# Kernel tuning notes

Hardware: AMD Instinct MI355X
Metric: run time of the kernel (lower is better)

The kernel has to match this reference:

```python
import jax, jax.numpy as jnp
import numpy as np

D = 512      # feature_bins
DK = 64      # d_k = d_v
H = 8        # n_heads
EPS = 1e-5


def setup_inputs() -> dict:
    key = jax.random.key(0)
    ks = jax.random.split(key, 12)
    B, S = 4, 2048
    s = 1.0 / np.sqrt(D)
    inp = {
        "Q": jax.random.normal(ks[0], (B, S, D), jnp.float32),
        "K": jax.random.normal(ks[1], (B, S, D), jnp.float32),
        "V": jax.random.normal(ks[2], (B, S, D), jnp.float32),
        # nn.Linear params: weight [out, in], bias [out]
        "Wq": jax.random.normal(ks[3], (H * DK, D), jnp.float32) * s,
        "bq": jnp.zeros((H * DK,), jnp.float32),
        "Wk": jax.random.normal(ks[4], (H * DK, D), jnp.float32) * s,
        "bk": jnp.zeros((H * DK,), jnp.float32),
        "Wv": jax.random.normal(ks[5], (H * DK, D), jnp.float32) * s,
        "bv": jnp.zeros((H * DK,), jnp.float32),
        "Wo": jax.random.normal(ks[6], (D, H * DK), jnp.float32) * s,
        "bo": jnp.zeros((D,), jnp.float32),
        "gamma": jnp.ones((D,), jnp.float32),
        "beta": jnp.zeros((D,), jnp.float32),
    }
    return inp


def _layernorm(x, gamma, beta):
    mu = jnp.mean(x, axis=-1, keepdims=True)
    var = jnp.mean(jnp.square(x - mu), axis=-1, keepdims=True)
    return (x - mu) * jax.lax.rsqrt(var + EPS) * gamma + beta


def reference(Q, K, V, Wq, bq, Wk, bk, Wv, bv, Wo, bo, gamma, beta):
    B, S, _ = Q.shape
    residual = Q
    # projections -> [B, H, S, DK]
    q = (Q @ Wq.T + bq).reshape(B, S, H, DK).transpose(0, 2, 1, 3)
    k = (K @ Wk.T + bk).reshape(B, S, H, DK).transpose(0, 2, 1, 3)
    v = (V @ Wv.T + bv).reshape(B, S, H, DK).transpose(0, 2, 1, 3)
    # NOTE: original code has NO 1/sqrt(d_k) scaling
    scores = jnp.einsum("bhqd,bhkd->bhqk", q, k)
    attn = jax.nn.softmax(scores, axis=-1)
    context = jnp.einsum("bhqk,bhkd->bhqd", attn, v)
    context = context.transpose(0, 2, 1, 3).reshape(B, S, H * DK)
    output = context @ Wo.T + bo
    out = _layernorm(output + residual, gamma, beta)
    return (out, attn)
```

## Files before the change

### kernel.cpp

```cpp
#include <hip/hip_runtime.h>

#define NB 4
#define NS 2048
#define ND 512
#define NH 8
#define NDK 64
#define LN_EPS 1e-5f
#define SCLAMP 115.0f
#define LOG2E 1.44269504f

typedef __attribute__((ext_vector_type(8))) short short8;
typedef __attribute__((ext_vector_type(4))) short s16x4;
typedef __attribute__((ext_vector_type(4))) float f32x4;

__device__ inline short f2bf(float x) {
    unsigned u = __builtin_bit_cast(unsigned, x);
    unsigned r = (u + 0x7FFFu + ((u >> 16) & 1u)) >> 16;
    return (short)r;
}
__device__ inline float bf2f(short h) {
    unsigned u = ((unsigned)(unsigned short)h) << 16;
    return __builtin_bit_cast(float, u);
}
__device__ inline unsigned splitT(float x) {
    unsigned u = __builtin_bit_cast(unsigned, x);
    unsigned h = u >> 16;
    float r = x - bf2f((short)h);
    unsigned l = __builtin_bit_cast(unsigned, r) >> 16;
    return (h & 0xFFFFu) | (l << 16);
}

__device__ inline int swzS(int row, int b8) {
    return row * 64 + (((b8) * 8) ^ ((row & 7) << 3));
}
__device__ inline int swz4(int row, int g4) {
    return row * 64 + ((((g4 >> 1)) * 8) ^ ((row & 7) << 3)) + (g4 & 1) * 4;
}

__global__ __launch_bounds__(256) void k_projm_all(
    const float* __restrict__ Qx, const float* __restrict__ Kx,
    const float* __restrict__ Vx,
    const float* __restrict__ Wq, const float* __restrict__ bq,
    const float* __restrict__ Wk, const float* __restrict__ bk,
    const float* __restrict__ Wv, const float* __restrict__ bv,
    short* __restrict__ qh, short* __restrict__ ql,
    short* __restrict__ kh, short* __restrict__ kl,
    short* __restrict__ vtb)
{
    __shared__ short WsH[8192], WsL[8192];
    const int which = blockIdx.z;
    const float* X    = which == 0 ? Qx : (which == 1 ? Kx : Vx);
    const float* W    = which == 0 ? Wq : (which == 1 ? Wk : Wv);
    const float* bias = which == 0 ? bq : (which == 1 ? bk : bv);
    short* outh       = which == 0 ? qh : (which == 1 ? kh : vtb);
    short* outl       = which == 0 ? ql : kl;

    const int tid = threadIdx.x;
    const int w = tid >> 6, lane = tid & 63;
    const int lr = lane & 15, lg = lane >> 4;
    const int row0 = blockIdx.y * 64;
    const int col0 = blockIdx.x * 128;
    const int xrow = row0 + w * 16 + lr;

    f32x4 acc[8] = {};

    float4 wb[8], ab[4];
#pragma unroll
    for (int i = 0; i < 8; ++i) {
        int idx = tid + 256 * i, wrow = idx >> 4, g4 = idx & 15;
        wb[i] = *(const float4*)&W[(size_t)(col0 + wrow) * ND + g4 * 4];
    }
#pragma unroll
    for (int ks = 0; ks < 2; ++ks) {
        ab[2*ks+0] = *(const float4*)&X[(size_t)xrow * ND + ks * 32 + lg * 8];
        ab[2*ks+1] = *(const float4*)&X[(size_t)xrow * ND + ks * 32 + lg * 8 + 4];
    }

    for (int kc = 0; kc < 8; ++kc) {
        __syncthreads();
#pragma unroll
        for (int i = 0; i < 8; ++i) {
            int idx = tid + 256 * i, wrow = idx >> 4, g4 = idx & 15;
            s16x4 hv, lv;
            unsigned p0 = splitT(wb[i].x), p1 = splitT(wb[i].y);
            unsigned p2 = splitT(wb[i].z), p3 = splitT(wb[i].w);
            hv[0] = (short)p0; lv[0] = (short)(p0 >> 16);
            hv[1] = (short)p1; lv[1] = (short)(p1 >> 16);
            hv[2] = (short)p2; lv[2] = (short)(p2 >> 16);
            hv[3] = (short)p3; lv[3] = (short)(p3 >> 16);
            int off = swz4(wrow, g4);
            *(s16x4*)&WsH[off] = hv;
            *(s16x4*)&WsL[off] = lv;
        }
        __syncthreads();

        short8 ah[2], al[2];
#pragma unroll
        for (int ks = 0; ks < 2; ++ks) {
#pragma unroll
            for (int j = 0; j < 4; ++j) {
                unsigned p = splitT(ab[2*ks][j]);
                ah[ks][j] = (short)p; al[ks][j] = (short)(p >> 16);
            }
#pragma unroll
            for (int j = 0; j < 4; ++j) {
                unsigned p = splitT(ab[2*ks+1][j]);
                ah[ks][4+j] = (short)p; al[ks][4+j] = (short)(p >> 16);
            }
        }

        if (kc < 7) {
            const int kn = (kc + 1) * 64;
#pragma unroll
            for (int i = 0; i < 8; ++i) {
                int idx = tid + 256 * i, wrow = idx >> 4, g4 = idx & 15;
                wb[i] = *(const float4*)&W[(size_t)(col0 + wrow) * ND + kn + g4 * 4];
            }
#pragma unroll
            for (int ks = 0; ks < 2; ++ks) {
                ab[2*ks+0] = *(const float4*)&X[(size_t)xrow * ND + kn + ks * 32 + lg * 8];
                ab[2*ks+1] = *(const float4*)&X[(size_t)xrow * ND + kn + ks * 32 + lg * 8 + 4];
            }
        }

#pragma unroll
        for (int cs = 0; cs < 8; ++cs)
#pragma unroll
            for (int ks = 0; ks < 2; ++ks) {
                short8 fh = *(const short8*)&WsH[swzS(cs * 16 + lr, ks * 4 + lg)];
                short8 fl = *(const short8*)&WsL[swzS(cs * 16 + lr, ks * 4 + lg)];
                acc[cs] = __builtin_amdgcn_mfma_f32_16x16x32_bf16(ah[ks], fh, acc[cs], 0, 0, 0);
                acc[cs] = __builtin_amdgcn_mfma_f32_16x16x32_bf16(ah[ks], fl, acc[cs], 0, 0, 0);
                acc[cs] = __builtin_amdgcn_mfma_f32_16x16x32_bf16(al[ks], fh, acc[cs], 0, 0, 0);
            }
    }

#pragma unroll
    for (int cs = 0; cs < 8; ++cs) {
        int c = col0 + cs * 16 + lr;
        int h_ = c >> 6, dk = c & (NDK - 1);
        float bv = bias[c];
#pragma unroll
        for (int r = 0; r < 4; ++r) {
            int gr = row0 + w * 16 + lg * 4 + r;
            int b_ = gr >> 11, s_ = gr & (NS - 1);
            float x = acc[cs][r] + bv;
            if (which == 0) x *= LOG2E;
            if (which != 2) {
                size_t idx = (((size_t)b_ * NH + h_) * NS + s_) * NDK + dk;
                short hb = f2bf(x);
                outh[idx] = hb;
                outl[idx] = f2bf(x - bf2f(hb));
            } else {
                size_t idx = (((size_t)b_ * NH + h_) * NDK + dk) * NS + s_;
                outh[idx] = f2bf(x);
            }
        }
    }
}

__device__ inline void att_decode2(int wg, int& bh, int& rt) {
    rt = (wg >> 3) & 15;
    bh = (wg & 7) + ((wg >> 7) << 3);
}

__global__ __launch_bounds__(256) void k_att(
    const short* __restrict__ qh, const short* __restrict__ ql,
    const short* __restrict__ kh, const short* __restrict__ kl,
    const short* __restrict__ vtb,
    short* __restrict__ ctxb, float* __restrict__ attn)
{
    __shared__ short KsH[4096], KsL[4096], Vs[4096];
    __shared__ short plbf[4][32][72];
    const int tid = threadIdx.x;
    const int w = tid >> 6, lane = tid & 63;
    const int lr = lane & 15, lg = lane >> 4;
    int bh, rt;
    att_decode2(blockIdx.x, bh, rt);
    const int row0 = rt * 128 + w * 16;
    const size_t base = (size_t)bh * NS * NDK;
    const short* vb = vtb + (size_t)bh * NDK * NS;
    float* ab = attn + (size_t)bh * NS * NS;
    const int srow0 = tid >> 3, sb8 = tid & 7;
    const int srow1 = srow0 + 32;

    short8 ah[2][2], al[2][2];
#pragma unroll
    for (int st = 0; st < 2; ++st)
#pragma unroll
        for (int ks = 0; ks < 2; ++ks) {
            size_t idx = base + (size_t)(row0 + st * 64 + lr) * NDK + ks * 32 + lg * 8;
            ah[st][ks] = *(const short8*)&qh[idx];
            al[st][ks] = *(const short8*)&ql[idx];
        }

    float lsum[2][4] = {};
    f32x4 vacc[2][4] = {};

    short8 nh0, nh1, nl0, nl1, nv0, nv1;
    {
        nh0 = *(const short8*)&kh[base + (size_t)(srow0) * NDK + sb8 * 8];
        nh1 = *(const short8*)&kh[base + (size_t)(srow1) * NDK + sb8 * 8];
        nl0 = *(const short8*)&kl[base + (size_t)(srow0) * NDK + sb8 * 8];
        nl1 = *(const short8*)&kl[base + (size_t)(srow1) * NDK + sb8 * 8];
        nv0 = *(const short8*)&vb[(size_t)srow0 * NS + sb8 * 8];
        nv1 = *(const short8*)&vb[(size_t)srow1 * NS + sb8 * 8];
    }

    for (int c = 0; c < 32; ++c) {
        short8 ch0 = nh0, ch1 = nh1, cl0 = nl0, cl1 = nl1, cv0 = nv0, cv1 = nv1;
        __syncthreads();
        *(short8*)&KsH[swzS(srow0, sb8)] = ch0;
        *(short8*)&KsH[swzS(srow1, sb8)] = ch1;
        *(short8*)&KsL[swzS(srow0, sb8)] = cl0;
        *(short8*)&KsL[swzS(srow1, sb8)] = cl1;
        *(short8*)&Vs[swzS(srow0, sb8)] = cv0;
        *(short8*)&Vs[swzS(srow1, sb8)] = cv1;
        __syncthreads();

        if (c < 31) {
            const int coln = (c + 1) * 64;
            nh0 = *(const short8*)&kh[base + (size_t)(coln + srow0) * NDK + sb8 * 8];
            nh1 = *(const short8*)&kh[base + (size_t)(coln + srow1) * NDK + sb8 * 8];
            nl0 = *(const short8*)&kl[base + (size_t)(coln + srow0) * NDK + sb8 * 8];
            nl1 = *(const short8*)&kl[base + (size_t)(coln + srow1) * NDK + sb8 * 8];
            nv0 = *(const short8*)&vb[(size_t)srow0 * NS + coln + sb8 * 8];
            nv1 = *(const short8*)&vb[(size_t)srow1 * NS + coln + sb8 * 8];
        }

        f32x4 sa[2][4] = {};
#pragma unroll
        for (int cs = 0; cs < 4; ++cs)
#pragma unroll
            for (int ks = 0; ks < 2; ++ks) {
                short8 fh = *(const short8*)&KsH[swzS(cs * 16 + lr, ks * 4 + lg)];
                short8 fl = *(const short8*)&KsL[swzS(cs * 16 + lr, ks * 4 + lg)];
#pragma unroll
                for (int st = 0; st < 2; ++st) {
                    sa[st][cs] = __builtin_amdgcn_mfma_f32_16x16x32_bf16(ah[st][ks], fh, sa[st][cs], 0, 0, 0);
                    sa[st][cs] = __builtin_amdgcn_mfma_f32_16x16x32_bf16(ah[st][ks], fl, sa[st][cs], 0, 0, 0);
                    sa[st][cs] = __builtin_amdgcn_mfma_f32_16x16x32_bf16(al[st][ks], fh, sa[st][cs], 0, 0, 0);
                }
            }

#pragma unroll
        for (int st = 0; st < 2; ++st)
#pragma unroll
            for (int cs = 0; cs < 4; ++cs)
#pragma unroll
                for (int r = 0; r < 4; ++r) {
                    float e = __builtin_amdgcn_exp2f(fminf(sa[st][cs][r], SCLAMP));
                    lsum[st][r] += e;
                    plbf[w][st * 16 + lg * 4 + r][cs * 16 + lr] = f2bf(e);
                }

#pragma unroll
        for (int k2 = 0; k2 < 2; ++k2) {
            short8 pa0 = *(const short8*)&plbf[w][lr][k2 * 32 + lg * 8];
            short8 pa1 = *(const short8*)&plbf[w][16 + lr][k2 * 32 + lg * 8];
#pragma unroll
            for (int d = 0; d < 4; ++d) {
                short8 vf = *(const short8*)&Vs[swzS(d * 16 + lr, k2 * 4 + lg)];
                vacc[0][d] = __builtin_amdgcn_mfma_f32_16x16x32_bf16(pa0, vf, vacc[0][d], 0, 0, 0);
                vacc[1][d] = __builtin_amdgcn_mfma_f32_16x16x32_bf16(pa1, vf, vacc[1][d], 0, 0, 0);
            }
        }
    }

#pragma unroll
    for (int st = 0; st < 2; ++st)
#pragma unroll
        for (int r = 0; r < 4; ++r)
#pragma unroll
            for (int off = 1; off < 16; off <<= 1)
                lsum[st][r] += __shfl_xor(lsum[st][r], off);

    float iL[2][4];
#pragma unroll
    for (int st = 0; st < 2; ++st)
#pragma unroll
        for (int r = 0; r < 4; ++r) iL[st][r] = 1.0f / lsum[st][r];

    const int b_ = bh >> 3, h_ = bh & 7;
#pragma unroll
    for (int st = 0; st < 2; ++st)
#pragma unroll
        for (int d = 0; d < 4; ++d)
#pragma unroll
            for (int r = 0; r < 4; ++r) {
                int row = row0 + st * 64 + lg * 4 + r;
                ctxb[((size_t)b_ * NS + row) * ND + h_ * NDK + d * 16 + lr] =
                    f2bf(vacc[st][d][r] * iL[st][r]);
            }

    {
        nh0 = *(const short8*)&kh[base + (size_t)(srow0) * NDK + sb8 * 8];
        nh1 = *(const short8*)&kh[base + (size_t)(srow1) * NDK + sb8 * 8];
        nl0 = *(const short8*)&kl[base + (size_t)(srow0) * NDK + sb8 * 8];
        nl1 = *(const short8*)&kl[base + (size_t)(srow1) * NDK + sb8 * 8];
    }

    for (int c = 0; c < 32; ++c) {
        short8 ch0 = nh0, ch1 = nh1, cl0 = nl0, cl1 = nl1;
        __syncthreads();
        *(short8*)&KsH[swzS(srow0, sb8)] = ch0;
        *(short8*)&KsH[swzS(srow1, sb8)] = ch1;
        *(short8*)&KsL[swzS(srow0, sb8)] = cl0;
        *(short8*)&KsL[swzS(srow1, sb8)] = cl1;
        __syncthreads();

        if (c < 31) {
            const int coln = (c + 1) * 64;
            nh0 = *(const short8*)&kh[base + (size_t)(coln + srow0) * NDK + sb8 * 8];
            nh1 = *(const short8*)&kh[base + (size_t)(coln + srow1) * NDK + sb8 * 8];
            nl0 = *(const short8*)&kl[base + (size_t)(coln + srow0) * NDK + sb8 * 8];
            nl1 = *(const short8*)&kl[base + (size_t)(coln + srow1) * NDK + sb8 * 8];
        }

        const int col0 = c * 64;
        f32x4 sa[2][4] = {};
#pragma unroll
        for (int cs = 0; cs < 4; ++cs)
#pragma unroll
            for (int ks = 0; ks < 2; ++ks) {
                short8 fh = *(const short8*)&KsH[swzS(cs * 16 + lr, ks * 4 + lg)];
                short8 fl = *(const short8*)&KsL[swzS(cs * 16 + lr, ks * 4 + lg)];
#pragma unroll
                for (int st = 0; st < 2; ++st) {
                    sa[st][cs] = __builtin_amdgcn_mfma_f32_16x16x32_bf16(ah[st][ks], fh, sa[st][cs], 0, 0, 0);
                    sa[st][cs] = __builtin_amdgcn_mfma_f32_16x16x32_bf16(ah[st][ks], fl, sa[st][cs], 0, 0, 0);
                    sa[st][cs] = __builtin_amdgcn_mfma_f32_16x16x32_bf16(al[st][ks], fh, sa[st][cs], 0, 0, 0);
                }
            }

#pragma unroll
        for (int st = 0; st < 2; ++st)
#pragma unroll
            for (int cs = 0; cs < 4; ++cs)
#pragma unroll
                for (int r = 0; r < 4; ++r) {
                    float p = __builtin_amdgcn_exp2f(fminf(sa[st][cs][r], SCLAMP)) * iL[st][r];
                    ab[(size_t)(row0 + st * 64 + lg * 4 + r) * NS + col0 + cs * 16 + lr] = p;
                }
    }
}

__global__ __launch_bounds__(256) void k_outproj_m(
    const short* __restrict__ Xc, const float* __restrict__ W,
    const float* __restrict__ bias, const float* __restrict__ Qin,
    float* __restrict__ out)
{
    __shared__ short WsH[8192], WsL[8192];
    const int tid = threadIdx.x;
    const int w = tid >> 6, lane = tid & 63;
    const int lr = lane & 15, lg = lane >> 4;
    const int row0 = blockIdx.y * 64;
    const int col0 = blockIdx.x * 128;
    const int xrow = row0 + w * 16 + lr;

    f32x4 acc[8] = {};

    float4 wb[8];
    short8 abn[2];
#pragma unroll
    for (int i = 0; i < 8; ++i) {
        int idx = tid + 256 * i, wrow = idx >> 4, g4 = idx & 15;
        wb[i] = *(const float4*)&W[(size_t)(col0 + wrow) * ND + g4 * 4];
    }
#pragma unroll
    for (int ks = 0; ks < 2; ++ks)
        abn[ks] = *(const short8*)&Xc[(size_t)xrow * ND + ks * 32 + lg * 8];

    for (int kc = 0; kc < 8; ++kc) {
        __syncthreads();
#pragma unroll
        for (int i = 0; i < 8; ++i) {
            int idx = tid + 256 * i, wrow = idx >> 4, g4 = idx & 15;
            s16x4 hv, lv;
            unsigned p0 = splitT(wb[i].x), p1 = splitT(wb[i].y);
            unsigned p2 = splitT(wb[i].z), p3 = splitT(wb[i].w);
            hv[0] = (short)p0; lv[0] = (short)(p0 >> 16);
            hv[1] = (short)p1; lv[1] = (short)(p1 >> 16);
            hv[2] = (short)p2; lv[2] = (short)(p2 >> 16);
            hv[3] = (short)p3; lv[3] = (short)(p3 >> 16);
            int off = swz4(wrow, g4);
            *(s16x4*)&WsH[off] = hv;
            *(s16x4*)&WsL[off] = lv;
        }
        __syncthreads();

        short8 ah[2] = { abn[0], abn[1] };

        if (kc < 7) {
            const int kn = (kc + 1) * 64;
#pragma unroll
            for (int i = 0; i < 8; ++i) {
                int idx = tid + 256 * i, wrow = idx >> 4, g4 = idx & 15;
                wb[i] = *(const float4*)&W[(size_t)(col0 + wrow) * ND + kn + g4 * 4];
            }
#pragma unroll
            for (int ks = 0; ks < 2; ++ks)
                abn[ks] = *(const short8*)&Xc[(size_t)xrow * ND + kn + ks * 32 + lg * 8];
        }

#pragma unroll
        for (int cs = 0; cs < 8; ++cs)
#pragma unroll
            for (int ks = 0; ks < 2; ++ks) {
                short8 fh = *(const short8*)&WsH[swzS(cs * 16 + lr, ks * 4 + lg)];
                short8 fl = *(const short8*)&WsL[swzS(cs * 16 + lr, ks * 4 + lg)];
                acc[cs] = __builtin_amdgcn_mfma_f32_16x16x32_bf16(ah[ks], fh, acc[cs], 0, 0, 0);
                acc[cs] = __builtin_amdgcn_mfma_f32_16x16x32_bf16(ah[ks], fl, acc[cs], 0, 0, 0);
            }
    }

#pragma unroll
    for (int cs = 0; cs < 8; ++cs) {
        int c = col0 + cs * 16 + lr;
        float bv = bias[c];
#pragma unroll
        for (int r = 0; r < 4; ++r) {
            int gr = row0 + w * 16 + lg * 4 + r;
            float res = Qin[(size_t)gr * ND + c];
            out[(size_t)gr * ND + c] = acc[cs][r] + bv + res;
        }
    }
}

__global__ __launch_bounds__(256) void k_ln(
    float* __restrict__ out, const float* __restrict__ gamma,
    const float* __restrict__ beta)
{
    const int tid = threadIdx.x;
    float* p = out + (size_t)blockIdx.x * ND;
    float2 v = *(const float2*)&p[tid * 2];

    float s = v.x + v.y;
#pragma unroll
    for (int off = 32; off > 0; off >>= 1) s += __shfl_xor(s, off);
    __shared__ float red1[4];
    __shared__ float red2[4];
    if ((tid & 63) == 0) red1[tid >> 6] = s;
    __syncthreads();
    const float mu = (red1[0] + red1[1] + red1[2] + red1[3]) * (1.0f / ND);

    float dx = v.x - mu, dy = v.y - mu;
    float q = dx * dx + dy * dy;
#pragma unroll
    for (int off = 32; off > 0; off >>= 1) q += __shfl_xor(q, off);
    if ((tid & 63) == 0) red2[tid >> 6] = q;
    __syncthreads();
    const float var = (red2[0] + red2[1] + red2[2] + red2[3]) * (1.0f / ND);
    const float inv = rsqrtf(var + LN_EPS);

    float2 g = *(const float2*)&gamma[tid * 2];
    float2 be = *(const float2*)&beta[tid * 2];
    float2 o = { dx * inv * g.x + be.x, dy * inv * g.y + be.y };
    *(float2*)&p[tid * 2] = o;
}

extern "C" void kernel_launch(void* const* d_in, const int* in_sizes, int n_in,
                              void* d_out, int out_size, void* d_ws, size_t ws_size,
                              hipStream_t stream)
{
    const float* Q    = (const float*)d_in[0];
    const float* K    = (const float*)d_in[1];
    const float* V    = (const float*)d_in[2];
    const float* Wq   = (const float*)d_in[3];
    const float* bq   = (const float*)d_in[4];
    const float* Wk   = (const float*)d_in[5];
    const float* bk   = (const float*)d_in[6];
    const float* Wv   = (const float*)d_in[7];
    const float* bv   = (const float*)d_in[8];
    const float* Wo   = (const float*)d_in[9];
    const float* bo   = (const float*)d_in[10];
    const float* gam  = (const float*)d_in[11];
    const float* bet  = (const float*)d_in[12];

    float* out  = (float*)d_out;
    float* attn = out + (size_t)NB * NS * ND;

    const size_t QKV = (size_t)NB * NH * NS * NDK;
    short* qh   = (short*)d_ws;
    short* ql   = qh + QKV;
    short* kh   = ql + QKV;
    short* kl   = kh + QKV;
    short* vtb  = kl + QKV;
    short* ctxb = vtb + QKV;

    dim3 blk(256);

    dim3 gP(ND / 128, (NB * NS) / 64, 3);
    k_projm_all<<<gP, blk, 0, stream>>>(Q, K, V, Wq, bq, Wk, bk, Wv, bv,
                                        qh, ql, kh, kl, vtb);

    dim3 gAtt((NS / 128) * NB * NH);
    k_att<<<gAtt, blk, 0, stream>>>(qh, ql, kh, kl, vtb, ctxb, attn);

    dim3 gO(ND / 128, (NB * NS) / 64);
    k_outproj_m<<<gO, blk, 0, stream>>>(ctxb, Wo, bo, Q, out);

    k_ln<<<dim3(NB * NS), blk, 0, stream>>>(out, gam, bet);
}
```

Measured before the change: 307.2 us.

## Double-buffer K/V shared tiles in attention and drop exp clamp

Converts the attention kernel's K/V shared-memory tiles to double buffers with prefetch two chunks ahead. This removes one barrier per iteration, so global loads and LDS stores overlap MFMA compute. It also removes the fminf clamp before exp2, which saves an instruction per score but risks overflow if scores exceed the fp32 exp range. The double buffers add LDS usage and may lower occupancy.

```diff
diff --git a/kernel.cpp b/kernel.cpp
--- a/kernel.cpp
+++ b/kernel.cpp
@@ -6,7 +6,6 @@
 #define NH 8
 #define NDK 64
 #define LN_EPS 1e-5f
-#define SCLAMP 115.0f
 #define LOG2E 1.44269504f
 
 typedef __attribute__((ext_vector_type(8))) short short8;
@@ -170,7 +169,7 @@
     const short* __restrict__ vtb,
     short* __restrict__ ctxb, float* __restrict__ attn)
 {
-    __shared__ short KsH[4096], KsL[4096], Vs[4096];
+    __shared__ short KsH[2][4096], KsL[2][4096], Vs[2][4096];
     __shared__ short plbf[4][32][72];
     const int tid = threadIdx.x;
     const int w = tid >> 6, lane = tid & 63;
@@ -183,6 +182,7 @@
     float* ab = attn + (size_t)bh * NS * NS;
     const int srow0 = tid >> 3, sb8 = tid & 7;
     const int srow1 = srow0 + 32;
+    const int so0 = swzS(srow0, sb8), so1 = swzS(srow1, sb8);
 
     short8 ah[2][2], al[2][2];
 #pragma unroll
@@ -198,28 +198,32 @@
     f32x4 vacc[2][4] = {};
 
     short8 nh0, nh1, nl0, nl1, nv0, nv1;
-    {
-        nh0 = *(const short8*)&kh[base + (size_t)(srow0) * NDK + sb8 * 8];
-        nh1 = *(const short8*)&kh[base + (size_t)(srow1) * NDK + sb8 * 8];
-        nl0 = *(const short8*)&kl[base + (size_t)(srow0) * NDK + sb8 * 8];
-        nl1 = *(const short8*)&kl[base + (size_t)(srow1) * NDK + sb8 * 8];
-        nv0 = *(const short8*)&vb[(size_t)srow0 * NS + sb8 * 8];
-        nv1 = *(const short8*)&vb[(size_t)srow1 * NS + sb8 * 8];
-    }
+    nh0 = *(const short8*)&kh[base + (size_t)(srow0) * NDK + sb8 * 8];
+    nh1 = *(const short8*)&kh[base + (size_t)(srow1) * NDK + sb8 * 8];
+    nl0 = *(const short8*)&kl[base + (size_t)(srow0) * NDK + sb8 * 8];
+    nl1 = *(const short8*)&kl[base + (size_t)(srow1) * NDK + sb8 * 8];
+    nv0 = *(const short8*)&vb[(size_t)srow0 * NS + sb8 * 8];
+    nv1 = *(const short8*)&vb[(size_t)srow1 * NS + sb8 * 8];
+    *(short8*)&KsH[0][so0] = nh0;  *(short8*)&KsH[0][so1] = nh1;
+    *(short8*)&KsL[0][so0] = nl0;  *(short8*)&KsL[0][so1] = nl1;
+    *(short8*)&Vs[0][so0]  = nv0;  *(short8*)&Vs[0][so1]  = nv1;
+    nh0 = *(const short8*)&kh[base + (size_t)(64 + srow0) * NDK + sb8 * 8];
+    nh1 = *(const short8*)&kh[base + (size_t)(64 + srow1) * NDK + sb8 * 8];
+    nl0 = *(const short8*)&kl[base + (size_t)(64 + srow0) * NDK + sb8 * 8];
+    nl1 = *(const short8*)&kl[base + (size_t)(64 + srow1) * NDK + sb8 * 8];
+    nv0 = *(const short8*)&vb[(size_t)srow0 * NS + 64 + sb8 * 8];
+    nv1 = *(const short8*)&vb[(size_t)srow1 * NS + 64 + sb8 * 8];
 
     for (int c = 0; c < 32; ++c) {
-        short8 ch0 = nh0, ch1 = nh1, cl0 = nl0, cl1 = nl1, cv0 = nv0, cv1 = nv1;
+        const int cur = c & 1, nxt = cur ^ 1;
         __syncthreads();
-        *(short8*)&KsH[swzS(srow0, sb8)] = ch0;
-        *(short8*)&KsH[swzS(srow1, sb8)] = ch1;
-        *(short8*)&KsL[swzS(srow0, sb8)] = cl0;
-        *(short8*)&KsL[swzS(srow1, sb8)] = cl1;
-        *(short8*)&Vs[swzS(srow0, sb8)] = cv0;
-        *(short8*)&Vs[swzS(srow1, sb8)] = cv1;
-        __syncthreads();
-
         if (c < 31) {
-            const int coln = (c + 1) * 64;
+            *(short8*)&KsH[nxt][so0] = nh0;  *(short8*)&KsH[nxt][so1] = nh1;
+            *(short8*)&KsL[nxt][so0] = nl0;  *(short8*)&KsL[nxt][so1] = nl1;
+            *(short8*)&Vs[nxt][so0]  = nv0;  *(short8*)&Vs[nxt][so1]  = nv1;
+        }
+        if (c < 30) {
+            const int coln = (c + 2) * 64;
             nh0 = *(const short8*)&kh[base + (size_t)(coln + srow0) * NDK + sb8 * 8];
             nh1 = *(const short8*)&kh[base + (size_t)(coln + srow1) * NDK + sb8 * 8];
             nl0 = *(const short8*)&kl[base + (size_t)(coln + srow0) * NDK + sb8 * 8];
@@ -233,8 +237,8 @@
         for (int cs = 0; cs < 4; ++cs)
 #pragma unroll
             for (int ks = 0; ks < 2; ++ks) {
-                short8 fh = *(const short8*)&KsH[swzS(cs * 16 + lr, ks * 4 + lg)];
-                short8 fl = *(const short8*)&KsL[swzS(cs * 16 + lr, ks * 4 + lg)];
+                short8 fh = *(const short8*)&KsH[cur][swzS(cs * 16 + lr, ks * 4 + lg)];
+                short8 fl = *(const short8*)&KsL[cur][swzS(cs * 16 + lr, ks * 4 + lg)];
 #pragma unroll
                 for (int st = 0; st < 2; ++st) {
                     sa[st][cs] = __builtin_amdgcn_mfma_f32_16x16x32_bf16(ah[st][ks], fh, sa[st][cs], 0, 0, 0);
@@ -249,7 +253,7 @@
             for (int cs = 0; cs < 4; ++cs)
 #pragma unroll
                 for (int r = 0; r < 4; ++r) {
-                    float e = __builtin_amdgcn_exp2f(fminf(sa[st][cs][r], SCLAMP));
+                    float e = __builtin_amdgcn_exp2f(sa[st][cs][r]);
                     lsum[st][r] += e;
                     plbf[w][st * 16 + lg * 4 + r][cs * 16 + lr] = f2bf(e);
                 }
@@ -260,7 +264,7 @@
             short8 pa1 = *(const short8*)&plbf[w][16 + lr][k2 * 32 + lg * 8];
 #pragma unroll
             for (int d = 0; d < 4; ++d) {
-                short8 vf = *(const short8*)&Vs[swzS(d * 16 + lr, k2 * 4 + lg)];
+                short8 vf = *(const short8*)&Vs[cur][swzS(d * 16 + lr, k2 * 4 + lg)];
                 vacc[0][d] = __builtin_amdgcn_mfma_f32_16x16x32_bf16(pa0, vf, vacc[0][d], 0, 0, 0);
                 vacc[1][d] = __builtin_amdgcn_mfma_f32_16x16x32_bf16(pa1, vf, vacc[1][d], 0, 0, 0);
             }
@@ -293,24 +297,27 @@
                     f2bf(vacc[st][d][r] * iL[st][r]);
             }
 
-    {
-        nh0 = *(const short8*)&kh[base + (size_t)(srow0) * NDK + sb8 * 8];
-        nh1 = *(const short8*)&kh[base + (size_t)(srow1) * NDK + sb8 * 8];
-        nl0 = *(const short8*)&kl[base + (size_t)(srow0) * NDK + sb8 * 8];
-        nl1 = *(const short8*)&kl[base + (size_t)(srow1) * NDK + sb8 * 8];
-    }
+    nh0 = *(const short8*)&kh[base + (size_t)(srow0) * NDK + sb8 * 8];
+    nh1 = *(const short8*)&kh[base + (size_t)(srow1) * NDK + sb8 * 8];
+    nl0 = *(const short8*)&kl[base + (size_t)(srow0) * NDK + sb8 * 8];
+    nl1 = *(const short8*)&kl[base + (size_t)(srow1) * NDK + sb8 * 8];
+    __syncthreads();
+    *(short8*)&KsH[0][so0] = nh0;  *(short8*)&KsH[0][so1] = nh1;
+    *(short8*)&KsL[0][so0] = nl0;  *(short8*)&KsL[0][so1] = nl1;
+    nh0 = *(const short8*)&kh[base + (size_t)(64 + srow0) * NDK + sb8 * 8];
+    nh1 = *(const short8*)&kh[base + (size_t)(64 + srow1) * NDK + sb8 * 8];
+    nl0 = *(const short8*)&kl[base + (size_t)(64 + srow0) * NDK + sb8 * 8];
+    nl1 = *(const short8*)&kl[base + (size_t)(64 + srow1) * NDK + sb8 * 8];
 
     for (int c = 0; c < 32; ++c) {
-        short8 ch0 = nh0, ch1 = nh1, cl0 = nl0, cl1 = nl1;
+        const int cur = c & 1, nxt = cur ^ 1;
         __syncthreads();
-        *(short8*)&KsH[swzS(srow0, sb8)] = ch0;
-        *(short8*)&KsH[swzS(srow1, sb8)] = ch1;
-        *(short8*)&KsL[swzS(srow0, sb8)] = cl0;
-        *(short8*)&KsL[swzS(srow1, sb8)] = cl1;
-        __syncthreads();
-
         if (c < 31) {
-            const int coln = (c + 1) * 64;
+            *(short8*)&KsH[nxt][so0] = nh0;  *(short8*)&KsH[nxt][so1] = nh1;
+            *(short8*)&KsL[nxt][so0] = nl0;  *(short8*)&KsL[nxt][so1] = nl1;
+        }
+        if (c < 30) {
+            const int coln = (c + 2) * 64;
             nh0 = *(const short8*)&kh[base + (size_t)(coln + srow0) * NDK + sb8 * 8];
             nh1 = *(const short8*)&kh[base + (size_t)(coln + srow1) * NDK + sb8 * 8];
             nl0 = *(const short8*)&kl[base + (size_t)(coln + srow0) * NDK + sb8 * 8];
@@ -323,8 +330,8 @@
         for (int cs = 0; cs < 4; ++cs)
 #pragma unroll
             for (int ks = 0; ks < 2; ++ks) {
-                short8 fh = *(const short8*)&KsH[swzS(cs * 16 + lr, ks * 4 + lg)];
-                short8 fl = *(const short8*)&KsL[swzS(cs * 16 + lr, ks * 4 + lg)];
+                short8 fh = *(const short8*)&KsH[cur][swzS(cs * 16 + lr, ks * 4 + lg)];
+                short8 fl = *(const short8*)&KsL[cur][swzS(cs * 16 + lr, ks * 4 + lg)];
 #pragma unroll
                 for (int st = 0; st < 2; ++st) {
                     sa[st][cs] = __builtin_amdgcn_mfma_f32_16x16x32_bf16(ah[st][ks], fh, sa[st][cs], 0, 0, 0);
@@ -339,7 +346,7 @@
             for (int cs = 0; cs < 4; ++cs)
 #pragma unroll
                 for (int r = 0; r < 4; ++r) {
-                    float p = __builtin_amdgcn_exp2f(fminf(sa[st][cs][r], SCLAMP)) * iL[st][r];
+                    float p = __builtin_amdgcn_exp2f(sa[st][cs][r]) * iL[st][r];
                     ab[(size_t)(row0 + st * 64 + lg * 4 + r) * NS + col0 + cs * 16 + lr] = p;
                 }
     }
```

Result: no change. 309.0 us (+0.6%).
